# Optimization experiments

Measured on AMD Instinct MI355X. Metric: run time of the kernel, lower is better.

Reference implementation:

```python
import jax, jax.numpy as jnp
import numpy as np

DIM = 4096
N_HEADS = 32
N_KV_HEADS = 8
HEAD_DIM = DIM // N_HEADS      # 128
N_REP = N_HEADS // N_KV_HEADS  # 4
B, S = 2, 2048
THETA = 10000.0


def _rope_tables(seq_len, head_dim):
    # standard llama2.c freqs: [1, S, 1, head_dim//2]
    freqs = 1.0 / (THETA ** (np.arange(0, head_dim, 2, dtype=np.float32) / head_dim))
    t = np.arange(seq_len, dtype=np.float32)
    ang = np.outer(t, freqs)  # [S, head_dim//2]
    cos = jnp.asarray(np.cos(ang))[None, :, None, :]
    sin = jnp.asarray(np.sin(ang))[None, :, None, :]
    return cos, sin


def setup_inputs() -> dict:
    key = jax.random.key(0)
    ks = jax.random.split(key, 5)
    x = jax.random.normal(ks[0], (B, S, DIM), dtype=jnp.float32)
    freqs_cos, freqs_sin = _rope_tables(S, HEAD_DIM)
    scale = 1.0 / np.sqrt(DIM)
    wq = jax.random.normal(ks[1], (DIM, N_HEADS * HEAD_DIM), dtype=jnp.float32) * scale
    wk = jax.random.normal(ks[2], (DIM, N_KV_HEADS * HEAD_DIM), dtype=jnp.float32) * scale
    wv = jax.random.normal(ks[3], (DIM, N_KV_HEADS * HEAD_DIM), dtype=jnp.float32) * scale
    wo = jax.random.normal(ks[4], (N_HEADS * HEAD_DIM, DIM), dtype=jnp.float32) * scale
    return {"x": x, "freqs_cos": freqs_cos, "freqs_sin": freqs_sin,
            "wq": wq, "wk": wk, "wv": wv, "wo": wo}


def _apply_rotary(t, cos, sin):
    # t: [B, S, H, head_dim]; cos/sin: [1, S, 1, head_dim//2]
    b, s, h, d = t.shape
    tr = t.reshape(b, s, h, d // 2, 2)
    t_r, t_i = tr[..., 0], tr[..., 1]
    out_r = t_r * cos - t_i * sin
    out_i = t_r * sin + t_i * cos
    return jnp.stack([out_r, out_i], axis=-1).reshape(b, s, h, d)


def reference(x, freqs_cos, freqs_sin, wq, wk, wv, wo):
    b, s, _ = x.shape
    q = (x @ wq).reshape(b, s, N_HEADS, HEAD_DIM)
    k = (x @ wk).reshape(b, s, N_KV_HEADS, HEAD_DIM)
    v = (x @ wv).reshape(b, s, N_KV_HEADS, HEAD_DIM)
    q = _apply_rotary(q, freqs_cos, freqs_sin)
    k = _apply_rotary(k, freqs_cos, freqs_sin)
    # GQA: repeat kv heads to match q heads
    k = jnp.repeat(k, N_REP, axis=2)  # [b, s, H, hd]
    v = jnp.repeat(v, N_REP, axis=2)
    # NOTE: source calls SDPA with attn_mask=None and no is_causal -> non-causal
    scores = jnp.einsum('bqhd,bkhd->bhqk', q, k) / jnp.sqrt(
        jnp.asarray(HEAD_DIM, dtype=q.dtype))
    attn = jax.nn.softmax(scores, axis=-1)
    out = jnp.einsum('bhqk,bkhd->bqhd', attn, v)
    out = out.reshape(b, s, N_HEADS * HEAD_DIM)
    return out @ wo
```

## Files before the change

### kernel.cpp

```cpp
#include <hip/hip_runtime.h>
#include <cstdint>


typedef __attribute__((ext_vector_type(8))) short short8;
typedef __attribute__((ext_vector_type(4))) float f32x4;
typedef __attribute__((ext_vector_type(16))) float f32x16;

__device__ __forceinline__ float bf2f(unsigned short u) {
  union { unsigned int i; float f; } v; v.i = ((unsigned int)u) << 16; return v.f;
}
__device__ __forceinline__ unsigned short f2bf(float f) {
  union { float f; unsigned int i; } v; v.f = f;
  unsigned int r = v.i + 0x7fffu + ((v.i >> 16) & 1u);
  return (unsigned short)(r >> 16);
}

__device__ __forceinline__ void gload_lds16(const void* g, void* lds) {
  __builtin_amdgcn_global_load_lds(
      (const __attribute__((address_space(1))) unsigned int*)g,
      (__attribute__((address_space(3))) unsigned int*)lds, 16, 0, 0);
}

__device__ __forceinline__ unsigned int cvtpk_bf16(float lo, float hi) {
  unsigned int r;
  asm("v_cvt_pk_bf16_f32 %0, %1, %2" : "=v"(r) : "v"(lo), "v"(hi));
  return r;
}
__device__ __forceinline__ void pl32swap(unsigned int& a, unsigned int& b) {
  asm("v_permlane32_swap_b32 %0, %1" : "+v"(a), "+v"(b));
}


__global__ __launch_bounds__(256) void cast_bf16(const float* __restrict__ src,
                                                 unsigned short* __restrict__ dst) {
  size_t i = (size_t)blockIdx.x * 256 + threadIdx.x;
  float4 v = ((const float4*)src)[i];
  ushort4 o; o.x = f2bf(v.x); o.y = f2bf(v.y); o.z = f2bf(v.z); o.w = f2bf(v.w);
  ((ushort4*)dst)[i] = o;
}

__global__ __launch_bounds__(256) void transpose_cast(const float* __restrict__ src,
                                                      unsigned short* __restrict__ dst,
                                                      int R, int C) {
  __shared__ float tile[32][33];
  int c0 = blockIdx.x * 32, r0 = blockIdx.y * 32;
  int tx = threadIdx.x & 31, ty = threadIdx.x >> 5;
#pragma unroll
  for (int j = 0; j < 4; ++j)
    tile[ty + j * 8][tx] = src[(size_t)(r0 + ty + j * 8) * C + c0 + tx];
  __syncthreads();
#pragma unroll
  for (int j = 0; j < 4; ++j)
    dst[(size_t)(c0 + ty + j * 8) * R + r0 + tx] = f2bf(tile[tx][ty + j * 8]);
}

__global__ __launch_bounds__(256) void rope_k(unsigned short* __restrict__ qkv,
                                              const float* __restrict__ cosT,
                                              const float* __restrict__ sinT) {
  int idx = blockIdx.x * 256 + threadIdx.x;
  int t = idx / 640;
  int cb = (idx - t * 640) * 8;
  int s = t & 2047;
  int j0 = (cb & 127) >> 1;
  unsigned short* p = qkv + (size_t)t * 6144 + cb;
  uint4 u = *(const uint4*)p;
  float4 c4 = *(const float4*)&cosT[s * 64 + j0];
  float4 s4 = *(const float4*)&sinT[s * 64 + j0];
  auto rot = [](unsigned int& uu, float c, float sn) {
    float re = bf2f((unsigned short)(uu & 0xffffu));
    float im = bf2f((unsigned short)(uu >> 16));
    float nr = re * c - im * sn;
    float ni = re * sn + im * c;
    uu = (unsigned int)f2bf(nr) | ((unsigned int)f2bf(ni) << 16);
  };
  rot(u.x, c4.x, s4.x); rot(u.y, c4.y, s4.y);
  rot(u.z, c4.z, s4.z); rot(u.w, c4.w, s4.w);
  *(uint4*)p = u;
}

__global__ __launch_bounds__(256) void transpose_v(const unsigned short* __restrict__ qkv,
                                                   unsigned short* __restrict__ vt) {
  __shared__ unsigned short tile[32][33];
  int bk = blockIdx.z;
  int s0 = blockIdx.x * 32, d0 = blockIdx.y * 32;
  int tx = threadIdx.x & 31, ty = threadIdx.x >> 5;
  int b = bk >> 3, kvh = bk & 7;
#pragma unroll
  for (int j = 0; j < 4; ++j)
    tile[ty + j * 8][tx] =
        qkv[(size_t)(b * 2048 + s0 + ty + j * 8) * 6144 + 5120 + kvh * 128 + d0 + tx];
  __syncthreads();
#pragma unroll
  for (int j = 0; j < 4; ++j)
    vt[(size_t)(bk * 128 + d0 + ty + j * 8) * 2048 + s0 + tx] = tile[tx][ty + j * 8];
}


#define GBAR() asm volatile("s_barrier" ::: "memory")
#define GVM6() asm volatile("s_waitcnt vmcnt(6)" ::: "memory")

#define GLDA(buf, mh)                                                                   \
  do {                                                                                  \
    _Pragma("unroll") for (int m_ = 0; m_ < 4; ++m_)                                    \
    _Pragma("unroll") for (int ks_ = 0; ks_ < 2; ++ks_)                                 \
      a[m_][ks_] = *(const short8*)&smem[buf][0]                                        \
          [(wm * 128 + (mh) * 64 + m_ * 16 + lr) * 64 + (((ks_ * 4 + lg) ^ (lr & 7)) << 3)]; \
  } while (0)

#define GLDB(bf_, buf, nh)                                                              \
  do {                                                                                  \
    _Pragma("unroll") for (int n_ = 0; n_ < 2; ++n_)                                    \
    _Pragma("unroll") for (int ks_ = 0; ks_ < 2; ++ks_)                                 \
      bf_[n_][ks_] = *(const short8*)&smem[buf][1]                                      \
          [(wn * 64 + (nh) * 32 + n_ * 16 + lr) * 64 + (((ks_ * 4 + lg) ^ (lr & 7)) << 3)]; \
  } while (0)

#define GMM(bf_, mh, nh)                                                                \
  do {                                                                                  \
    __builtin_amdgcn_s_setprio(1);                                                      \
    _Pragma("unroll") for (int ks_ = 0; ks_ < 2; ++ks_)                                 \
    _Pragma("unroll") for (int m_ = 0; m_ < 4; ++m_)                                    \
    _Pragma("unroll") for (int n_ = 0; n_ < 2; ++n_)                                    \
      acc[(mh) * 4 + m_][(nh) * 2 + n_] = __builtin_amdgcn_mfma_f32_16x16x32_bf16(      \
          a[m_][ks_], bf_[n_][ks_], acc[(mh) * 4 + m_][(nh) * 2 + n_], 0, 0, 0);        \
    __builtin_amdgcn_s_setprio(0);                                                      \
  } while (0)

#define GSTG(half, buf, tile)                                                           \
  do {                                                                                  \
    _Pragma("unroll") for (int t2_ = 0; t2_ < 2; ++t2_)                                 \
      gload_lds16(srcp[half][t2_] + ((size_t)(tile) << 6),                              \
                  &smem[buf][(half) >> 1][dsto[half][t2_]]);                            \
  } while (0)

template <typename OutT>
__global__ __launch_bounds__(512) void gemm256(const unsigned short* __restrict__ A,
                                               const unsigned short* __restrict__ B,
                                               OutT* __restrict__ C,
                                               int M, int N, int K) {
  __shared__ unsigned short smem[2][2][16384];
  const int nxc = N >> 8;
  const int nwg = gridDim.x;
  const int bid = blockIdx.x;
  const int swz = (bid & 7) * (nwg >> 3) + (bid >> 3);
  const int n0 = (swz % nxc) * 256, m0 = (swz / nxc) * 256;
  const int tid = threadIdx.x, w = tid >> 6, l = tid & 63;
  const int wm = w >> 2, wn = w & 3;
  const int lr = l & 15, lg = l >> 4;
  const int NT = K >> 6;

  const int lsub = l >> 3, lgr = l & 7;
  const int sg = (lgr ^ lsub) << 3;
  const unsigned short* srcp[4][2];
  int dsto[4][2];
#pragma unroll
  for (int t2 = 0; t2 < 2; ++t2) {
    int lb = t2 * 64 + w * 8;
    int pa0 = (lb & 63) + ((lb >> 6) << 7);
    int pb0 = (lb & 31) + ((lb >> 5) << 6);
    srcp[0][t2] = A + (size_t)(m0 + pa0 + lsub) * K + sg;       dsto[0][t2] = pa0 * 64;
    srcp[1][t2] = A + (size_t)(m0 + pa0 + 64 + lsub) * K + sg;  dsto[1][t2] = (pa0 + 64) * 64;
    srcp[2][t2] = B + (size_t)(n0 + pb0 + lsub) * K + sg;       dsto[2][t2] = pb0 * 64;
    srcp[3][t2] = B + (size_t)(n0 + pb0 + 32 + lsub) * K + sg;  dsto[3][t2] = (pb0 + 32) * 64;
  }

  f32x4 acc[8][4] = {};
  short8 a[4][2], b0f[2][2], b1f[2][2];

  GSTG(0, 0, 0); GSTG(2, 0, 0); GSTG(3, 0, 0); GSTG(1, 0, 0);
  GSTG(0, 1, 1); GSTG(2, 1, 1); GSTG(3, 1, 1);
  GVM6();
  GBAR();

  for (int t = 0; t < NT / 2; ++t) {
    const int t1 = 2 * t + 1;
    const int t2a = (2 * t + 2 < NT) ? 2 * t + 2 : NT - 1;
    const int t2b = (2 * t + 3 < NT) ? 2 * t + 3 : NT - 1;
    GLDA(0, 0); GLDB(b0f, 0, 0);
    GSTG(1, 1, t1);
    GBAR(); GMM(b0f, 0, 0); GBAR();
    GLDB(b1f, 0, 1);
    GSTG(0, 0, t2a);
    GBAR(); GMM(b1f, 0, 1); GBAR();
    GLDA(0, 1);
    GSTG(2, 0, t2a);
    GBAR(); GMM(b0f, 1, 0); GBAR();
    GSTG(3, 0, t2a);
    GBAR(); GMM(b1f, 1, 1); GVM6(); GBAR();
    GLDA(1, 0); GLDB(b0f, 1, 0);
    GSTG(1, 0, t2a);
    GBAR(); GMM(b0f, 0, 0); GBAR();
    GLDB(b1f, 1, 1);
    GSTG(0, 1, t2b);
    GBAR(); GMM(b1f, 0, 1); GBAR();
    GLDA(1, 1);
    GSTG(2, 1, t2b);
    GBAR(); GMM(b0f, 1, 0); GBAR();
    GSTG(3, 1, t2b);
    GBAR(); GMM(b1f, 1, 1); GVM6(); GBAR();
  }

#pragma unroll
  for (int m = 0; m < 8; ++m)
#pragma unroll
    for (int n = 0; n < 4; ++n)
#pragma unroll
      for (int r = 0; r < 4; ++r) {
        int row = m0 + wm * 128 + m * 16 + lg * 4 + r;
        int col = n0 + wn * 64 + n * 16 + lr;
        float v = acc[m][n][r];
        if constexpr (sizeof(OutT) == 2)
          C[(size_t)row * N + col] = (OutT)f2bf(v);
        else
          C[(size_t)row * N + col] = v;
      }
}


__global__ __launch_bounds__(256, 2) void attn_k(const unsigned short* __restrict__ qkv,
                                                 const unsigned short* __restrict__ vt,
                                                 unsigned short* __restrict__ ctx) {
  __shared__ unsigned short Ks[2][64 * 128];
  __shared__ unsigned short Vs[2][128 * 64];
  const int bid = blockIdx.x;
  const int xcd = bid & 7, idx = bid >> 3;
  const int kvg = xcd * 2 + (idx >> 6);
  const int hg = (idx >> 4) & 3;
  const int qt = idx & 15;
  const int b = kvg >> 3, kvh = kvg & 7, h = kvh * 4 + hg;
  const int w = threadIdx.x >> 6, l = threadIdx.x & 63;
  const int lc = l & 31, hi = l >> 5;
  const size_t tok0 = (size_t)b * 2048;
  const int q0 = qt * 128 + w * 32;
  const float C2 = 0.12751744516557944f;
  const float THR = 4.0f / C2;

  const unsigned short* ksrc[4];
  const unsigned short* vsrc[4];
#pragma unroll
  for (int i = 0; i < 4; ++i) {
    int L = w * 256 + i * 64 + l;
    int krow = L >> 4, kc = L & 15;
    ksrc[i] = qkv + (tok0 + krow) * 6144 + 4096 + kvh * 128 + ((kc ^ (krow & 7)) << 3);
    int vrow = L >> 3, vc = L & 7;
    vsrc[i] = vt + (size_t)(kvg * 128 + vrow) * 2048 + ((vc ^ (vrow & 7)) << 3);
  }
  const int ldsBase = (w * 256) * 8;

  auto stage = [&](int bufi, int kv0s) {
#pragma unroll
    for (int i = 0; i < 4; ++i)
      gload_lds16(ksrc[i] + (size_t)kv0s * 6144, &Ks[bufi][ldsBase + i * 512]);
#pragma unroll
    for (int i = 0; i < 4; ++i)
      gload_lds16(vsrc[i] + kv0s, &Vs[bufi][ldsBase + i * 512]);
  };

  const unsigned short* Qb = qkv + (tok0 + q0 + lc) * 6144 + h * 128 + hi * 8;
  short8 qf[8];
#pragma unroll
  for (int dc = 0; dc < 8; ++dc) qf[dc] = *(const short8*)(Qb + dc * 16);

  f32x16 acc[4] = {};
  float m = -1e30f, lsum = 0.f;

  stage(0, 0);
  __syncthreads();

  int buf = 0;
  for (int kt = 0; kt < 32; ++kt) {
    if (kt < 31) stage(buf ^ 1, (kt + 1) * 64);
    const int swz = (lc & 7) << 3;
    f32x16 s0 = {}, s1 = {};
#pragma unroll
    for (int dc = 0; dc < 8; ++dc) {
      int cidx = ((dc * 2 + hi) << 3) ^ swz;
      short8 kf0 = *(const short8*)&Ks[buf][lc * 128 + cidx];
      short8 kf1 = *(const short8*)&Ks[buf][(lc + 32) * 128 + cidx];
      s0 = __builtin_amdgcn_mfma_f32_32x32x16_bf16(kf0, qf[dc], s0, 0, 0, 0);
      s1 = __builtin_amdgcn_mfma_f32_32x32x16_bf16(kf1, qf[dc], s1, 0, 0, 0);
    }
    float tm = fmaxf(s0[0], s1[0]);
#pragma unroll
    for (int r = 1; r < 16; ++r) tm = fmaxf(tm, fmaxf(s0[r], s1[r]));
    tm = fmaxf(tm, __shfl_xor(tm, 32, 64));
    if (__any(tm > m + THR)) {
      float mn = fmaxf(m, tm);
      float sc = __builtin_amdgcn_exp2f((m - mn) * C2);
      m = mn;
      lsum *= sc;
#pragma unroll
      for (int r = 0; r < 16; ++r) {
        float sr = __shfl(sc, (r & 3) + 8 * (r >> 2) + 4 * hi, 64);
#pragma unroll
        for (int dt = 0; dt < 4; ++dt) acc[dt][r] *= sr;
      }
    }
    float p[32];
    float ts = 0.f;
#pragma unroll
    for (int r = 0; r < 16; ++r) p[r] = __builtin_amdgcn_exp2f((s0[r] - m) * C2);
#pragma unroll
    for (int r = 0; r < 16; ++r) p[16 + r] = __builtin_amdgcn_exp2f((s1[r] - m) * C2);
#pragma unroll
    for (int r = 0; r < 32; ++r) ts += p[r];
    ts += __shfl_xor(ts, 32, 64);
    lsum += ts;
    short8 pa[4];
#pragma unroll
    for (int g = 0; g < 4; ++g) {
      unsigned int c0 = cvtpk_bf16(p[g * 8 + 0], p[g * 8 + 1]);
      unsigned int c1 = cvtpk_bf16(p[g * 8 + 2], p[g * 8 + 3]);
      unsigned int c2 = cvtpk_bf16(p[g * 8 + 4], p[g * 8 + 5]);
      unsigned int c3 = cvtpk_bf16(p[g * 8 + 6], p[g * 8 + 7]);
      pl32swap(c0, c2);
      pl32swap(c1, c3);
      union { unsigned int u[4]; short8 v; } t;
      t.u[0] = c0; t.u[1] = c1; t.u[2] = c2; t.u[3] = c3;
      pa[g] = t.v;
    }
#pragma unroll
    for (int dt = 0; dt < 4; ++dt) {
#pragma unroll
      for (int ks = 0; ks < 4; ++ks) {
        short8 vf = *(const short8*)&Vs[buf][(dt * 32 + lc) * 64 + ((((ks * 2 + hi) << 3) ^ swz))];
        acc[dt] = __builtin_amdgcn_mfma_f32_32x32x16_bf16(pa[ks], vf, acc[dt], 0, 0, 0);
      }
    }
    __syncthreads();
    buf ^= 1;
  }
  float rl = 1.0f / lsum;
#pragma unroll
  for (int r = 0; r < 16; ++r) {
    int crow = (r & 3) + 8 * (r >> 2) + 4 * hi;
    float rlr = __shfl(rl, crow, 64);
    unsigned short* cp = ctx + (tok0 + q0 + crow) * 4096 + h * 128 + lc;
#pragma unroll
    for (int dt = 0; dt < 4; ++dt) cp[dt * 32] = f2bf(acc[dt][r] * rlr);
  }
}


extern "C" void kernel_launch(void* const* d_in, const int* in_sizes, int n_in,
                              void* d_out, int out_size, void* d_ws, size_t ws_size,
                              hipStream_t stream) {
  const float* x  = (const float*)d_in[0];
  const float* fc = (const float*)d_in[1];
  const float* fs = (const float*)d_in[2];
  const float* wq = (const float*)d_in[3];
  const float* wk = (const float*)d_in[4];
  const float* wv = (const float*)d_in[5];
  const float* wo = (const float*)d_in[6];
  float* out = (float*)d_out;
  char* ws = (char*)d_ws;

  constexpr size_t SZ_WQKVT = (size_t)6144 * 4096 * 2;
  constexpr size_t SZ_WOT   = (size_t)4096 * 4096 * 2;
  constexpr size_t SZ_QKV   = (size_t)4096 * 6144 * 2;
  constexpr size_t SZ_VT    = (size_t)16 * 128 * 2048 * 2;

  unsigned short* wqkvT = (unsigned short*)ws;
  unsigned short* woT   = (unsigned short*)(ws + SZ_WQKVT);
  unsigned short* qkv   = (unsigned short*)(ws + SZ_WQKVT + SZ_WOT);
  unsigned short* vt    = (unsigned short*)(ws + SZ_WQKVT + SZ_WOT + SZ_QKV);
  unsigned short* xbf   = (unsigned short*)(ws + SZ_WQKVT + SZ_WOT + SZ_QKV + SZ_VT);
  unsigned short* ctx   = xbf;

  cast_bf16<<<16384, 256, 0, stream>>>(x, xbf);
  transpose_cast<<<dim3(128, 128), 256, 0, stream>>>(wq, wqkvT, 4096, 4096);
  transpose_cast<<<dim3(32, 128), 256, 0, stream>>>(wk, wqkvT + (size_t)4096 * 4096, 4096, 1024);
  transpose_cast<<<dim3(32, 128), 256, 0, stream>>>(wv, wqkvT + (size_t)5120 * 4096, 4096, 1024);
  transpose_cast<<<dim3(128, 128), 256, 0, stream>>>(wo, woT, 4096, 4096);

  gemm256<unsigned short><<<384, 512, 0, stream>>>(xbf, wqkvT, qkv, 4096, 6144, 4096);
  rope_k<<<10240, 256, 0, stream>>>(qkv, fc, fs);
  transpose_v<<<dim3(64, 4, 16), 256, 0, stream>>>(qkv, vt);
  attn_k<<<1024, 256, 0, stream>>>(qkv, vt, ctx);
  gemm256<float><<<256, 512, 0, stream>>>(ctx, woT, out, 4096, 4096, 4096);
}
```

Baseline: 545.4 us.

## Split QKV GEMM into Q and KV kernels to balance CU waves

Replaces the single 384-workgroup QKV projection GEMM with a 256-workgroup Q GEMM and a separate 256-workgroup KV GEMM using 128x256 tiles. This avoids a partial second wave of workgroups on the device. It also adds an XCD-aware tile mapping hardcoded to the problem's grid shape and an LDS wait hint before barriers. The cost is an extra kernel launch, a narrower tile for KV with less reuse, and a loss of generality in the tile mapping.

```diff
diff --git a/kernel.cpp b/kernel.cpp
--- a/kernel.cpp
+++ b/kernel.cpp
@@ -98,6 +98,8 @@
 
 #define GBAR() asm volatile("s_barrier" ::: "memory")
 #define GVM6() asm volatile("s_waitcnt vmcnt(6)" ::: "memory")
+#define GVM4() asm volatile("s_waitcnt vmcnt(4)" ::: "memory")
+#define GHINT() asm volatile("s_waitcnt lgkmcnt(8)" ::: "memory")
 
 #define GLDA(buf, mh)                                                                   \
   do {                                                                                  \
@@ -134,16 +136,15 @@
   } while (0)
 
 template <typename OutT>
-__global__ __launch_bounds__(512) void gemm256(const unsigned short* __restrict__ A,
-                                               const unsigned short* __restrict__ B,
-                                               OutT* __restrict__ C,
-                                               int M, int N, int K) {
-  __shared__ unsigned short smem[2][2][16384];
-  const int nxc = N >> 8;
-  const int nwg = gridDim.x;
+__device__ __forceinline__ void gemm256_body(const unsigned short* __restrict__ A,
+                                             const unsigned short* __restrict__ B,
+                                             OutT* __restrict__ C, int K, int ldc,
+                                             unsigned short (*smem)[2][16384]) {
   const int bid = blockIdx.x;
-  const int swz = (bid & 7) * (nwg >> 3) + (bid >> 3);
-  const int n0 = (swz % nxc) * 256, m0 = (swz / nxc) * 256;
+  const int xcd = bid & 7, ii = bid >> 3;
+  const int mt = (xcd & 3) * 4 + (ii & 3);
+  const int nt = (xcd >> 2) * 8 + (ii >> 2);
+  const int m0 = mt * 256, n0 = nt * 256;
   const int tid = threadIdx.x, w = tid >> 6, l = tid & 63;
   const int wm = w >> 2, wn = w & 3;
   const int lr = l & 15, lg = l >> 4;
@@ -178,6 +179,7 @@
     const int t2b = (2 * t + 3 < NT) ? 2 * t + 3 : NT - 1;
     GLDA(0, 0); GLDB(b0f, 0, 0);
     GSTG(1, 1, t1);
+    GHINT();
     GBAR(); GMM(b0f, 0, 0); GBAR();
     GLDB(b1f, 0, 1);
     GSTG(0, 0, t2a);
@@ -189,6 +191,7 @@
     GBAR(); GMM(b1f, 1, 1); GVM6(); GBAR();
     GLDA(1, 0); GLDB(b0f, 1, 0);
     GSTG(1, 0, t2a);
+    GHINT();
     GBAR(); GMM(b0f, 0, 0); GBAR();
     GLDB(b1f, 1, 1);
     GSTG(0, 1, t2b);
@@ -210,9 +213,140 @@
         int col = n0 + wn * 64 + n * 16 + lr;
         float v = acc[m][n][r];
         if constexpr (sizeof(OutT) == 2)
-          C[(size_t)row * N + col] = (OutT)f2bf(v);
+          C[(size_t)row * ldc + col] = (OutT)f2bf(v);
         else
-          C[(size_t)row * N + col] = v;
+          C[(size_t)row * ldc + col] = v;
+      }
+}
+
+__global__ __launch_bounds__(512) void gemm_qproj(const unsigned short* __restrict__ A,
+                                                  const unsigned short* __restrict__ B,
+                                                  unsigned short* __restrict__ C,
+                                                  int K, int ldc) {
+  __shared__ unsigned short smem[2][2][16384];
+  gemm256_body<unsigned short>(A, B, C, K, ldc, smem);
+}
+
+__global__ __launch_bounds__(512) void gemm_oproj(const unsigned short* __restrict__ A,
+                                                  const unsigned short* __restrict__ B,
+                                                  float* __restrict__ C,
+                                                  int K, int ldc) {
+  __shared__ unsigned short smem[2][2][16384];
+  gemm256_body<float>(A, B, C, K, ldc, smem);
+}
+
+
+#define KLDA(buf)                                                                       \
+  do {                                                                                  \
+    _Pragma("unroll") for (int m_ = 0; m_ < 4; ++m_)                                    \
+    _Pragma("unroll") for (int ks_ = 0; ks_ < 2; ++ks_)                                 \
+      a2[m_][ks_] = *(const short8*)&As2[buf]                                           \
+          [(wm * 64 + m_ * 16 + lr) * 64 + (((ks_ * 4 + lg) ^ (lr & 7)) << 3)];         \
+  } while (0)
+
+#define KLDB(bf_, buf, nh)                                                              \
+  do {                                                                                  \
+    _Pragma("unroll") for (int n_ = 0; n_ < 2; ++n_)                                    \
+    _Pragma("unroll") for (int ks_ = 0; ks_ < 2; ++ks_)                                 \
+      bf_[n_][ks_] = *(const short8*)&Bs2[buf]                                          \
+          [(wn * 64 + (nh) * 32 + n_ * 16 + lr) * 64 + (((ks_ * 4 + lg) ^ (lr & 7)) << 3)]; \
+  } while (0)
+
+#define KMM(bf_, nh)                                                                    \
+  do {                                                                                  \
+    __builtin_amdgcn_s_setprio(1);                                                      \
+    _Pragma("unroll") for (int ks_ = 0; ks_ < 2; ++ks_)                                 \
+    _Pragma("unroll") for (int m_ = 0; m_ < 4; ++m_)                                    \
+    _Pragma("unroll") for (int n_ = 0; n_ < 2; ++n_)                                    \
+      acc[m_][(nh) * 2 + n_] = __builtin_amdgcn_mfma_f32_16x16x32_bf16(                 \
+          a2[m_][ks_], bf_[n_][ks_], acc[m_][(nh) * 2 + n_], 0, 0, 0);                  \
+    __builtin_amdgcn_s_setprio(0);                                                      \
+  } while (0)
+
+#define KSTGA(buf, tile)                                                                \
+  do {                                                                                  \
+    _Pragma("unroll") for (int t2_ = 0; t2_ < 2; ++t2_)                                 \
+      gload_lds16(srcA[t2_] + ((size_t)(tile) << 6), &As2[buf][dstA[t2_]]);             \
+  } while (0)
+#define KSTGB0(buf, tile)                                                               \
+  do {                                                                                  \
+    _Pragma("unroll") for (int t2_ = 0; t2_ < 2; ++t2_)                                 \
+      gload_lds16(srcB0[t2_] + ((size_t)(tile) << 6), &Bs2[buf][dstB0[t2_]]);           \
+  } while (0)
+#define KSTGB1(buf, tile)                                                               \
+  do {                                                                                  \
+    _Pragma("unroll") for (int t2_ = 0; t2_ < 2; ++t2_)                                 \
+      gload_lds16(srcB1[t2_] + ((size_t)(tile) << 6), &Bs2[buf][dstB1[t2_]]);           \
+  } while (0)
+
+__global__ __launch_bounds__(512) void gemm_kvproj(const unsigned short* __restrict__ A,
+                                                   const unsigned short* __restrict__ B,
+                                                   unsigned short* __restrict__ C,
+                                                   int K, int ldc) {
+  __shared__ unsigned short As2[2][8192];
+  __shared__ unsigned short Bs2[2][16384];
+  const int bid = blockIdx.x;
+  const int xcd = bid & 7, ii = bid >> 3;
+  const int mt = (xcd & 3) * 8 + (ii & 7);
+  const int nt = (xcd >> 2) * 4 + (ii >> 3);
+  const int m0 = mt * 128, n0 = nt * 256;
+  const int tid = threadIdx.x, w = tid >> 6, l = tid & 63;
+  const int wm = w >> 2, wn = w & 3;
+  const int lr = l & 15, lg = l >> 4;
+  const int NT = K >> 6;
+
+  const int lsub = l >> 3, lgr = l & 7;
+  const int sg = (lgr ^ lsub) << 3;
+  const unsigned short* srcA[2];  int dstA[2];
+  const unsigned short* srcB0[2]; int dstB0[2];
+  const unsigned short* srcB1[2]; int dstB1[2];
+#pragma unroll
+  for (int t2 = 0; t2 < 2; ++t2) {
+    int ra = t2 * 64 + w * 8;
+    srcA[t2] = A + (size_t)(m0 + ra + lsub) * K + sg;            dstA[t2] = ra * 64;
+    int lb = t2 * 64 + w * 8;
+    int pb0 = (lb & 31) + ((lb >> 5) << 6);
+    srcB0[t2] = B + (size_t)(n0 + pb0 + lsub) * K + sg;          dstB0[t2] = pb0 * 64;
+    srcB1[t2] = B + (size_t)(n0 + pb0 + 32 + lsub) * K + sg;     dstB1[t2] = (pb0 + 32) * 64;
+  }
+
+  f32x4 acc[4][4] = {};
+  short8 a2[4][2], bb0[2][2], bb1[2][2];
+
+  KSTGA(0, 0); KSTGB0(0, 0); KSTGB1(0, 0);
+  KSTGA(1, 1); KSTGB0(1, 1);
+  GVM4();
+  GBAR();
+
+  for (int t = 0; t < NT / 2; ++t) {
+    const int t1 = 2 * t + 1;
+    const int t2a = (2 * t + 2 < NT) ? 2 * t + 2 : NT - 1;
+    const int t2b = (2 * t + 3 < NT) ? 2 * t + 3 : NT - 1;
+    KLDA(0); KLDB(bb0, 0, 0);
+    KSTGB1(1, t1);
+    GHINT();
+    GBAR(); KMM(bb0, 0); GBAR();
+    KLDB(bb1, 0, 1);
+    KSTGA(0, t2a); KSTGB0(0, t2a);
+    GBAR(); KMM(bb1, 1); GVM4(); GBAR();
+    KLDA(1); KLDB(bb0, 1, 0);
+    KSTGB1(0, t2a);
+    GHINT();
+    GBAR(); KMM(bb0, 0); GBAR();
+    KLDB(bb1, 1, 1);
+    KSTGA(1, t2b); KSTGB0(1, t2b);
+    GBAR(); KMM(bb1, 1); GVM4(); GBAR();
+  }
+
+#pragma unroll
+  for (int m = 0; m < 4; ++m)
+#pragma unroll
+    for (int n = 0; n < 4; ++n)
+#pragma unroll
+      for (int r = 0; r < 4; ++r) {
+        int row = m0 + wm * 64 + m * 16 + lg * 4 + r;
+        int col = n0 + wn * 64 + n * 16 + lr;
+        C[(size_t)row * ldc + col] = f2bf(acc[m][n][r]);
       }
 }
 
@@ -373,9 +507,10 @@
   transpose_cast<<<dim3(32, 128), 256, 0, stream>>>(wv, wqkvT + (size_t)5120 * 4096, 4096, 1024);
   transpose_cast<<<dim3(128, 128), 256, 0, stream>>>(wo, woT, 4096, 4096);
 
-  gemm256<unsigned short><<<384, 512, 0, stream>>>(xbf, wqkvT, qkv, 4096, 6144, 4096);
+  gemm_qproj<<<256, 512, 0, stream>>>(xbf, wqkvT, qkv, 4096, 6144);
+  gemm_kvproj<<<256, 512, 0, stream>>>(xbf, wqkvT + (size_t)4096 * 4096, qkv + 4096, 4096, 6144);
   rope_k<<<10240, 256, 0, stream>>>(qkv, fc, fs);
   transpose_v<<<dim3(64, 4, 16), 256, 0, stream>>>(qkv, vt);
   attn_k<<<1024, 256, 0, stream>>>(qkv, vt, ctx);
-  gemm256<float><<<256, 512, 0, stream>>>(ctx, woT, out, 4096, 4096, 4096);
-}
+  gemm_oproj<<<256, 512, 0, stream>>>(ctx, woT, out, 4096, 4096);
+}
```

Measured after the change: 526.9 us. 1.04x faster.
